# Kernel optimization log

Measured on AMD Instinct MI355X. Metric: run time of the kernel, lower is better.

## Reference

```python
import jax, jax.numpy as jnp
import numpy as np

B, N, D, K = 16, 1024, 512, 8
NUM_ITERS = 3
EPS = 1e-08
LN_EPS = 1e-05


def layer_norm(x, g, b):
    m = jnp.mean(x, axis=-1, keepdims=True)
    v = jnp.var(x, axis=-1, keepdims=True)
    return (x - m) * jax.lax.rsqrt(v + LN_EPS) * g + b


def setup_inputs() -> dict:
    key = jax.random.key(0)
    ks = jax.random.split(key, 8)
    s = 1.0 / np.sqrt(D)
    return {
        "embeddings": jax.random.normal(ks[0], (B, N, D), jnp.float32),
        "noise_init": jax.random.normal(ks[1], (B, K, D), jnp.float32),
        "noise_final": jax.random.normal(ks[2], (B, K, D), jnp.float32),
        "slots_mu": jax.random.normal(ks[3], (1, K, D), jnp.float32) * s,
        "slots_logsigma": jax.random.normal(ks[4], (1, K, D), jnp.float32) * s,
        "mixing_coeffs": jnp.ones((1, K), jnp.float32) / K,
        "Wk": jax.random.normal(ks[5], (D, D), jnp.float32) * s,
        "bk": jnp.zeros((D,), jnp.float32),
        "Wq": jax.random.normal(ks[6], (D, D), jnp.float32) * s,
        "bq": jnp.zeros((D,), jnp.float32),
        "Wv": jax.random.normal(ks[7], (D, D), jnp.float32) * s,
        "bv": jnp.zeros((D,), jnp.float32),
        "ln_g": jnp.ones((D,), jnp.float32),
        "ln_b": jnp.zeros((D,), jnp.float32),
    }


def reference(embeddings, noise_init, noise_final, slots_mu, slots_logsigma,
              mixing_coeffs, Wk, bk, Wq, bq, Wv, bv, ln_g, ln_b):
    b, n, d = embeddings.shape
    mixing = jnp.broadcast_to(mixing_coeffs, (b, K))           # [B,K]
    mu = jnp.broadcast_to(slots_mu, (b, K, d))                 # [B,K,D]
    sigma = jnp.exp(jnp.broadcast_to(slots_logsigma, (b, K, d)))
    slots = mu + sigma * noise_init                            # sampled slots

    x = layer_norm(embeddings, ln_g, ln_b)
    keys = x @ Wk + bk                                         # [B,N,D]
    values = x @ Wv + bv                                       # [B,N,D]
    # slots are never updated inside the loop, so queries are loop-invariant
    queries = slots @ Wq + bq                                  # [B,K,D]

    log2pi = jnp.float32(np.log(2.0 * np.pi))
    attn = None
    for _ in range(NUM_ITERS):
        diff = keys[:, :, None, :] - queries[:, None, :, :]    # [B,N,K,D]
        gll = -0.5 * jnp.sum(diff * diff / (sigma[:, None] ** 2 + EPS), axis=-1)  # [B,N,K]
        gll = (-0.5 * d * log2pi
               - 0.5 * jnp.sum(jnp.log(jnp.abs(sigma) + EPS), axis=-1)[:, None, :]
               + gll)
        attn = mixing[:, None, :] * gll                        # [B,N,K]
        attn = attn / jnp.sum(attn, axis=-1, keepdims=True)
        attn = attn / (jnp.sum(attn, axis=1, keepdims=True) + EPS)
        mu = jnp.einsum('bnk,bnd->bkd', attn, values)          # [B,K,D]
        diff2 = values[:, :, None, :] - mu[:, None, :, :]      # [B,N,K,D]
        sigma = jnp.einsum('bnk,bnkd->bkd', attn, diff2 * diff2)
        mixing = jnp.sum(attn, axis=1) / n

    sigma = jnp.maximum(jnp.abs(sigma), EPS)
    slots = mu + sigma * noise_final
    return slots, jnp.transpose(attn, (0, 2, 1))
```

## Files before the change

### kernel.cpp

```cpp
#include <hip/hip_runtime.h>
#include <math.h>

#define BB 16
#define NN 1024
#define DD 512
#define KK 8
#define EPS_ 1e-8f
#define LN_EPS_ 1e-5f
#define GLL_C0 (-470.4965290007924f)

typedef __attribute__((ext_vector_type(8))) short short8;
typedef __attribute__((ext_vector_type(4))) short short4v;
typedef __attribute__((ext_vector_type(4))) float f32x4;

static __device__ inline short f2bf(float f) {
    unsigned u = __builtin_bit_cast(unsigned, f);
    u = (u + 0x7fff + ((u >> 16) & 1)) >> 16;
    return (short)u;
}
static __device__ inline float bf2f(short s) {
    unsigned u = ((unsigned)(unsigned short)s) << 16;
    return __builtin_bit_cast(float, u);
}
static __device__ inline void gload16(const void* g, void* l) {
    __builtin_amdgcn_global_load_lds(
        (const __attribute__((address_space(1))) void*)g,
        (__attribute__((address_space(3))) void*)l, 16, 0, 0);
}

struct Params {
    const float *emb, *noise_init, *noise_final, *slots_mu, *slots_logsg,
                *mixing_co, *Wk, *bk, *Wq, *bq, *Wv, *bv, *ln_g, *ln_b;
    float *out;
    float *queries, *attn, *s1p, *s2p, *off, *mix16, *colsum;
    short *Abf, *E, *Vbf, *WtKV, *WqT, *slotbf, *F_bt;
};

__global__ __launch_bounds__(256) void k_pre(Params p)
{
    __shared__ __align__(16) short eb[4352];
    int u = blockIdx.x, tid = threadIdx.x;
    if (u < 4096) {
        int row  = u * 4 + (tid >> 6);
        int lane = tid & 63;
        const float* e = p.emb + (size_t)row * DD + lane * 8;
        float4 v0 = *(const float4*)e;
        float4 v1 = *(const float4*)(e + 4);
        float v[8] = {v0.x, v0.y, v0.z, v0.w, v1.x, v1.y, v1.z, v1.w};
        float s = 0.0f;
#pragma unroll
        for (int j = 0; j < 8; j++) s += v[j];
#pragma unroll
        for (int off = 32; off; off >>= 1) s += __shfl_xor(s, off);
        float m = s * (1.0f / DD);
        float vs = 0.0f;
#pragma unroll
        for (int j = 0; j < 8; j++) { float d = v[j] - m; vs = fmaf(d, d, vs); }
#pragma unroll
        for (int off = 32; off; off >>= 1) vs += __shfl_xor(vs, off);
        float rstd = rsqrtf(vs * (1.0f / DD) + LN_EPS_);

        float4 g0 = *(const float4*)&p.ln_g[lane * 8];
        float4 g1 = *(const float4*)&p.ln_g[lane * 8 + 4];
        float4 b0 = *(const float4*)&p.ln_b[lane * 8];
        float4 b1 = *(const float4*)&p.ln_b[lane * 8 + 4];
        float g[8] = {g0.x, g0.y, g0.z, g0.w, g1.x, g1.y, g1.z, g1.w};
        float bb[8] = {b0.x, b0.y, b0.z, b0.w, b1.x, b1.y, b1.z, b1.w};
        short8 o;
#pragma unroll
        for (int j = 0; j < 8; j++) o[j] = f2bf(fmaf((v[j] - m) * rstd, g[j], bb[j]));
        *(short8*)&p.Abf[(size_t)row * DD + lane * 8] = o;
    } else if (u < 4864) {
        int idx = u - 4096;
        int z = idx >> 8, rem = idx & 255;
        const float* W = (z == 0) ? p.Wk : (z == 1) ? p.Wv : p.Wq;
        short* T; int nbase;
        if (z < 2) { T = p.WtKV; nbase = z * 512; } else { T = p.WqT; nbase = 0; }
        int k0 = (rem & 15) * 32, n0 = (rem >> 4) * 32;
        int tx = tid & 31, ty = tid >> 5;
        float (*t)[33] = (float (*)[33])eb;
#pragma unroll
        for (int q = 0; q < 4; q++)
            t[ty + q * 8][tx] = W[(size_t)(k0 + ty + q * 8) * DD + n0 + tx];
        __syncthreads();
#pragma unroll
        for (int q = 0; q < 4; q++)
            T[(size_t)(nbase + n0 + ty + q * 8) * DD + k0 + tx] = f2bf(t[tx][ty + q * 8]);
    } else {
        int idx = u - 4864;
        int b = idx >> 3, k = idx & 7;
#pragma unroll
        for (int q = 0; q < 2; q++) {
            int d = tid + q * 256;
            float sg = expf(p.slots_logsg[k * DD + d]);
            float sl = fmaf(sg, p.noise_init[((size_t)(b * KK + k)) * DD + d],
                            p.slots_mu[k * DD + d]);
            p.slotbf[((size_t)(b * KK + k)) * DD + d] = f2bf(sl);
        }
    }
}

__global__ __launch_bounds__(256) void k_gemm(Params p)
{
    __shared__ __align__(16) short eb[128 * 128];
    int u = blockIdx.x, tid = threadIdx.x;
    int w = tid >> 6, l = tid & 63;
    int x = u & 7, by = u >> 3;
    int qmode = (by == 128);
    if (qmode && x >= 4) return;
    const short* A  = qmode ? p.slotbf : p.Abf + (size_t)by * 128 * DD;
    const short* Bt = qmode ? p.WqT : p.WtKV;
    int row0 = qmode ? 0 : by * 128;
    int col0 = x * 128;

    short* As = eb;
    short* Bs = eb + 8192;
    int sr = l >> 3;
    int sg_off = ((l & 7) ^ sr) * 8;
    int mq = (w & 1) * 64, nq = (w >> 1) * 64;
    int fr = l & 15;
    int orow = (l >> 4) * 4, ocol = l & 15;

    f32x4 acc[4][4] = {};
    for (int k0 = 0; k0 < DD; k0 += 64) {
        __syncthreads();
#pragma unroll
        for (int j = 0; j < 4; j++) {
            int rb = w * 32 + j * 8;
            int r  = rb + sr;
            gload16(A  + (size_t)r * DD + k0 + sg_off, &As[rb * 64 + l * 8]);
            gload16(Bt + (size_t)(col0 + r) * DD + k0 + sg_off, &Bs[rb * 64 + l * 8]);
        }
        __syncthreads();
#pragma unroll
        for (int kk = 0; kk < 2; kk++) {
            int g = kk * 4 + (l >> 4);
            short8 af[4], bfv[4];
#pragma unroll
            for (int mi = 0; mi < 4; mi++)
                af[mi] = *(const short8*)&As[(mq + mi * 16 + fr) * 64 + (g ^ (fr & 7)) * 8];
#pragma unroll
            for (int ni = 0; ni < 4; ni++)
                bfv[ni] = *(const short8*)&Bs[(nq + ni * 16 + fr) * 64 + (g ^ (fr & 7)) * 8];
#pragma unroll
            for (int mi = 0; mi < 4; mi++)
#pragma unroll
                for (int ni = 0; ni < 4; ni++)
                    acc[mi][ni] = __builtin_amdgcn_mfma_f32_16x16x32_bf16(
                        af[mi], bfv[ni], acc[mi][ni], 0, 0, 0);
        }
    }

    float bvv[4];
#pragma unroll
    for (int ni = 0; ni < 4; ni++) {
        int col = col0 + nq + ni * 16 + ocol;
        bvv[ni] = qmode ? p.bq[col] : (x < 4 ? p.bk[col] : p.bv[col - 512]);
    }

    __syncthreads();
    if (qmode) {
#pragma unroll
        for (int ni = 0; ni < 4; ni++) {
            int col = col0 + nq + ni * 16 + ocol;
#pragma unroll
            for (int mi = 0; mi < 4; mi++)
#pragma unroll
                for (int r = 0; r < 4; r++)
                    p.queries[(size_t)(mq + mi * 16 + orow + r) * DD + col] =
                        acc[mi][ni][r] + bvv[ni];
        }
    } else {
        int npass = (x < 4) ? 2 : 1;
        for (int pass = 0; pass < npass; pass++) {
#pragma unroll
            for (int mi = 0; mi < 4; mi++)
#pragma unroll
                for (int r = 0; r < 4; r++) {
                    int row = mq + mi * 16 + orow + r;
                    int sw = ((row >> 2) & 3) << 1;
#pragma unroll
                    for (int ni = 0; ni < 4; ni++) {
                        int colg = nq + ni * 16 + ocol;
                        float val = acc[mi][ni][r] + bvv[ni];
                        if (x < 4 && pass == 0) val = val * val;
                        eb[row * 128 + (((colg >> 3) ^ sw) * 8) + (colg & 7)] = f2bf(val);
                    }
                }
            __syncthreads();
#pragma unroll
            for (int i = 0; i < 8; i++) {
                int row = i * 16 + w * 4 + (l >> 4);
                int c = l & 15;
                int cc = c ^ (((row >> 2) & 3) << 1);
                short8 vv = *(const short8*)&eb[row * 128 + cc * 8];
                if (x < 4) {
                    size_t a = (size_t)(row0 + row) * 1024 +
                               (pass ? 512 + col0 : col0) + c * 8;
                    *(short8*)&p.E[a] = vv;
                } else {
                    *(short8*)&p.Vbf[(size_t)(row0 + row) * 512 +
                                     (col0 - 512) + c * 8] = vv;
                }
            }
            __syncthreads();
        }
    }
}

__global__ __launch_bounds__(256) void k_fprep0(Params p)
{
    __shared__ float red[512];
    int u = blockIdx.x, tid = threadIdx.x;
    int b = u >> 4, k = u & 15;
    short* Fr = p.F_bt + (size_t)(b * 16 + k) * 1024;
    if (k >= KK) {
        short4v zv = {0, 0, 0, 0};
        *(short4v*)&Fr[tid * 4] = zv;
        if (tid == 0) { p.off[b * 16 + k] = 0.0f; p.mix16[b * 16 + k] = 0.0f; }
        return;
    }
    float* rc = red;
    float* rl = red + 256;
    float c = 0.0f, ld = 0.0f;
#pragma unroll
    for (int q = 0; q < 2; q++) {
        int d = tid * 2 + q;
        float sg = expf(p.slots_logsg[k * DD + d]);
        float iv = 1.0f / (sg * sg + EPS_);
        float qv = p.queries[((size_t)(b * KK + k)) * DD + d];
        Fr[d]       = f2bf(-0.5f * iv);
        Fr[512 + d] = f2bf(qv * iv);
        c  = fmaf(qv * qv, iv, c);
        ld += logf(fabsf(sg) + EPS_);
    }
    rc[tid] = c; rl[tid] = ld;
    __syncthreads();
    for (int s = 128; s > 0; s >>= 1) {
        if (tid < s) { rc[tid] += rc[tid + s]; rl[tid] += rl[tid + s]; }
        __syncthreads();
    }
    if (tid == 0) {
        p.off[b * 16 + k]    = GLL_C0 - 0.5f * rl[0] - 0.5f * rc[0];
        p.mix16[b * 16 + k]  = p.mixing_co[k];
        p.colsum[b * KK + k] = 0.0f;
    }
}

__global__ __launch_bounds__(256) void k_gllmu(Params p)
{
    __shared__ float asml[64 * KK];
    int u = blockIdx.x, tid = threadIdx.x;
    int w = tid >> 6, l = tid & 63;
    int b = u >> 4, chunk = u & 15;
    int n0 = chunk * 64;
    int m0 = n0 + w * 16;

    const short* Ea = p.E + ((size_t)(b * NN + m0 + (l & 15))) * 1024 + (l >> 4) * 8;
    const short* Fa = p.F_bt + (size_t)(b * 16 + (l & 15)) * 1024 + (l >> 4) * 8;
    f32x4 acc = {};
#pragma unroll 8
    for (int j = 0; j < 32; j++) {
        short8 af = *(const short8*)&Ea[j * 32];
        short8 bf = *(const short8*)&Fa[j * 32];
        acc = __builtin_amdgcn_mfma_f32_16x16x32_bf16(af, bf, acc, 0, 0, 0);
    }
    int col = l & 15;
    int rloc = w * 16 + (l >> 4) * 4;
    float offv = p.off[b * 16 + col];
    float mixv = p.mix16[b * 16 + col];
    float a[4], den[4];
#pragma unroll
    for (int r = 0; r < 4; r++) {
        a[r] = mixv * (acc[r] + offv);
        den[r] = a[r];
    }
#pragma unroll
    for (int mask = 1; mask <= 8; mask <<= 1)
#pragma unroll
        for (int r = 0; r < 4; r++) den[r] += __shfl_xor(den[r], mask);
    float csl = 0.0f;
    if (col < KK) {
#pragma unroll
        for (int r = 0; r < 4; r++) {
            float vv = a[r] / den[r];
            asml[(rloc + r) * KK + col] = vv;
            p.attn[((size_t)(b * NN + n0 + rloc + r)) * KK + col] = vv;
            csl += vv;
        }
    }
    csl += __shfl_xor(csl, 16);
    csl += __shfl_xor(csl, 32);
    if (l < KK) atomicAdd(&p.colsum[b * KK + l], csl);

    __syncthreads();

    int d0 = tid * 2;
    float s1[2][KK] = {}, s2[2][KK] = {};
    const short* vb = p.Vbf + ((size_t)(b * NN + n0)) * DD + d0;
#pragma unroll 4
    for (int nn = 0; nn < 64; nn++) {
        short2 vs = *(const short2*)&vb[(size_t)nn * DD];
        float v0 = bf2f(vs.x), v1 = bf2f(vs.y);
        float v0q = v0 * v0, v1q = v1 * v1;
        float4 a0 = *(const float4*)&asml[nn * KK];
        float4 a1 = *(const float4*)&asml[nn * KK + 4];
        float aa[8] = {a0.x, a0.y, a0.z, a0.w, a1.x, a1.y, a1.z, a1.w};
#pragma unroll
        for (int k = 0; k < KK; k++) {
            s1[0][k] = fmaf(aa[k], v0, s1[0][k]);
            s2[0][k] = fmaf(aa[k], v0q, s2[0][k]);
            s1[1][k] = fmaf(aa[k], v1, s1[1][k]);
            s2[1][k] = fmaf(aa[k], v1q, s2[1][k]);
        }
    }
    size_t base = ((size_t)(b * 16 + chunk) * KK) * DD + d0;
#pragma unroll
    for (int k = 0; k < KK; k++) {
        *(float2*)&p.s1p[base + (size_t)k * DD] = make_float2(s1[0][k], s1[1][k]);
        *(float2*)&p.s2p[base + (size_t)k * DD] = make_float2(s2[0][k], s2[1][k]);
    }
}

__global__ __launch_bounds__(256) void k_fprep(Params p)
{
    __shared__ float red[512];
    int u = blockIdx.x, tid = threadIdx.x;
    int b = u >> 3, k = u & 7;
    float cs   = p.colsum[b * KK + k];
    float inv  = 1.0f / (cs + EPS_);
    float ssum = cs * inv;
    short* Fr = p.F_bt + (size_t)(b * 16 + k) * 1024;
    float* rc = red;
    float* rl = red + 256;
    float c = 0.0f, ld = 0.0f;
#pragma unroll
    for (int q = 0; q < 2; q++) {
        int d = tid * 2 + q;
        float s1 = 0.0f, s2 = 0.0f;
#pragma unroll
        for (int ns = 0; ns < 16; ns++) {
            size_t o = ((size_t)(b * 16 + ns) * KK + k) * DD + d;
            s1 += p.s1p[o];
            s2 += p.s2p[o];
        }
        float m  = s1 * inv;
        float sg = s2 * inv - m * m * (2.0f - ssum);
        float iv = 1.0f / (sg * sg + EPS_);
        float qv = p.queries[((size_t)(b * KK + k)) * DD + d];
        Fr[d]       = f2bf(-0.5f * iv);
        Fr[512 + d] = f2bf(qv * iv);
        c  = fmaf(qv * qv, iv, c);
        ld += logf(fabsf(sg) + EPS_);
    }
    rc[tid] = c; rl[tid] = ld;
    __syncthreads();
    for (int s = 128; s > 0; s >>= 1) {
        if (tid < s) { rc[tid] += rc[tid + s]; rl[tid] += rl[tid + s]; }
        __syncthreads();
    }
    if (tid == 0) {
        p.off[b * 16 + k]    = GLL_C0 - 0.5f * rl[0] - 0.5f * rc[0];
        p.mix16[b * 16 + k]  = ssum * (1.0f / NN);
        p.colsum[b * KK + k] = 0.0f;
    }
}

__global__ __launch_bounds__(256) void k_final(Params p)
{
    int u = blockIdx.x, tid = threadIdx.x;
    if (u < 256) {
        int gid = u * 256 + tid;
        int d = gid & 511;
        int k = (gid >> 9) & 7;
        int b = gid >> 12;
        float s1 = 0.0f, s2 = 0.0f;
#pragma unroll
        for (int ns = 0; ns < 16; ns++) {
            size_t o = ((size_t)(b * 16 + ns) * KK + k) * DD + d;
            s1 += p.s1p[o];
            s2 += p.s2p[o];
        }
        float cs   = p.colsum[b * KK + k];
        float inv  = 1.0f / (cs + EPS_);
        float ssum = cs * inv;
        float m    = s1 * inv;
        float sg   = s2 * inv - m * m * (2.0f - ssum);
        p.out[gid] = fmaf(fmaxf(fabsf(sg), EPS_), p.noise_final[gid], m);
    } else {
        int gid = (u - 256) * 256 + tid;
        int b = gid >> 13;
        int k = (gid >> 10) & 7;
        int n = gid & 1023;
        float cs = p.colsum[b * KK + k];
        p.out[BB * KK * DD + gid] =
            p.attn[((size_t)(b * NN + n)) * KK + k] / (cs + EPS_);
    }
}

extern "C" void kernel_launch(void* const* d_in, const int* in_sizes, int n_in,
                              void* d_out, int out_size, void* d_ws, size_t ws_size,
                              hipStream_t stream)
{
    Params pp;
    pp.emb         = (const float*)d_in[0];
    pp.noise_init  = (const float*)d_in[1];
    pp.noise_final = (const float*)d_in[2];
    pp.slots_mu    = (const float*)d_in[3];
    pp.slots_logsg = (const float*)d_in[4];
    pp.mixing_co   = (const float*)d_in[5];
    pp.Wk          = (const float*)d_in[6];
    pp.bk          = (const float*)d_in[7];
    pp.Wq          = (const float*)d_in[8];
    pp.bq          = (const float*)d_in[9];
    pp.Wv          = (const float*)d_in[10];
    pp.bv          = (const float*)d_in[11];
    pp.ln_g        = (const float*)d_in[12];
    pp.ln_b        = (const float*)d_in[13];
    pp.out         = (float*)d_out;

    float* ws = (float*)d_ws;
    pp.queries = ws;
    pp.attn    = pp.queries + BB * KK * DD;
    pp.s1p     = pp.attn + BB * NN * KK;
    pp.s2p     = pp.s1p + (size_t)BB * 16 * KK * DD;
    pp.off     = pp.s2p + (size_t)BB * 16 * KK * DD;
    pp.mix16   = pp.off + BB * 16;
    pp.colsum  = pp.mix16 + BB * 16;
    pp.Abf     = (short*)(pp.colsum + BB * KK);
    pp.E       = pp.Abf + (size_t)BB * NN * DD;
    pp.Vbf     = pp.E + (size_t)BB * NN * 1024;
    pp.WtKV    = pp.Vbf + (size_t)BB * NN * DD;
    pp.WqT     = pp.WtKV + (size_t)1024 * DD;
    pp.slotbf  = pp.WqT + (size_t)DD * DD;
    pp.F_bt    = pp.slotbf + (size_t)BB * KK * DD;

    k_pre<<<4992, 256, 0, stream>>>(pp);
    k_gemm<<<1032, 256, 0, stream>>>(pp);
    k_fprep0<<<256, 256, 0, stream>>>(pp);
    for (int it = 0; it < 3; it++) {
        k_gllmu<<<256, 256, 0, stream>>>(pp);
        if (it < 2) k_fprep<<<128, 256, 0, stream>>>(pp);
    }
    k_final<<<768, 256, 0, stream>>>(pp);
}
```

Before: 243.6 us.

## Double-buffer GEMM LDS tiles and split gll/mu kernel over more blocks

The projection GEMM now keeps two LDS buffers and issues the next K-tile's loads before computing on the current one, aiming to overlap global loads with MFMA work. The gll/mu kernel processes 32 rows per block instead of 64, with warp pairs splitting the 1024-long reduction and combining through shared memory. This doubles the block count for better GPU fill. In exchange, GEMM LDS use doubles (lower occupancy) and the downstream reductions read twice as many partial sums.

```diff
diff --git a/kernel.cpp b/kernel.cpp
--- a/kernel.cpp
+++ b/kernel.cpp
@@ -102,7 +102,7 @@
 
 __global__ __launch_bounds__(256) void k_gemm(Params p)
 {
-    __shared__ __align__(16) short eb[128 * 128];
+    __shared__ __align__(16) short smem[32768];
     int u = blockIdx.x, tid = threadIdx.x;
     int w = tid >> 6, l = tid & 63;
     int x = u & 7, by = u >> 3;
@@ -113,35 +113,42 @@
     int row0 = qmode ? 0 : by * 128;
     int col0 = x * 128;
 
-    short* As = eb;
-    short* Bs = eb + 8192;
     int sr = l >> 3;
     int sg_off = ((l & 7) ^ sr) * 8;
     int mq = (w & 1) * 64, nq = (w >> 1) * 64;
     int fr = l & 15;
     int orow = (l >> 4) * 4, ocol = l & 15;
 
+#define STAGE(buf, k0)                                                        \
+    {                                                                         \
+        short* As_ = smem + (buf) * 8192;                                     \
+        short* Bs_ = smem + 16384 + (buf) * 8192;                             \
+        _Pragma("unroll")                                                     \
+        for (int j = 0; j < 4; j++) {                                         \
+            int rb = w * 32 + j * 8;                                          \
+            int r  = rb + sr;                                                 \
+            gload16(A  + (size_t)r * DD + (k0) + sg_off, &As_[rb * 64 + l * 8]);   \
+            gload16(Bt + (size_t)(col0 + r) * DD + (k0) + sg_off, &Bs_[rb * 64 + l * 8]); \
+        }                                                                     \
+    }
+
     f32x4 acc[4][4] = {};
-    for (int k0 = 0; k0 < DD; k0 += 64) {
-        __syncthreads();
-#pragma unroll
-        for (int j = 0; j < 4; j++) {
-            int rb = w * 32 + j * 8;
-            int r  = rb + sr;
-            gload16(A  + (size_t)r * DD + k0 + sg_off, &As[rb * 64 + l * 8]);
-            gload16(Bt + (size_t)(col0 + r) * DD + k0 + sg_off, &Bs[rb * 64 + l * 8]);
-        }
-        __syncthreads();
+    STAGE(0, 0);
+    __syncthreads();
+    for (int i = 0; i < 8; i++) {
+        if (i < 7) STAGE((i + 1) & 1, (i + 1) * 64);
+        const short* As_ = smem + (i & 1) * 8192;
+        const short* Bs_ = smem + 16384 + (i & 1) * 8192;
 #pragma unroll
         for (int kk = 0; kk < 2; kk++) {
             int g = kk * 4 + (l >> 4);
             short8 af[4], bfv[4];
 #pragma unroll
             for (int mi = 0; mi < 4; mi++)
-                af[mi] = *(const short8*)&As[(mq + mi * 16 + fr) * 64 + (g ^ (fr & 7)) * 8];
+                af[mi] = *(const short8*)&As_[(mq + mi * 16 + fr) * 64 + (g ^ (fr & 7)) * 8];
 #pragma unroll
             for (int ni = 0; ni < 4; ni++)
-                bfv[ni] = *(const short8*)&Bs[(nq + ni * 16 + fr) * 64 + (g ^ (fr & 7)) * 8];
+                bfv[ni] = *(const short8*)&Bs_[(nq + ni * 16 + fr) * 64 + (g ^ (fr & 7)) * 8];
 #pragma unroll
             for (int mi = 0; mi < 4; mi++)
 #pragma unroll
@@ -149,7 +156,9 @@
                     acc[mi][ni] = __builtin_amdgcn_mfma_f32_16x16x32_bf16(
                         af[mi], bfv[ni], acc[mi][ni], 0, 0, 0);
         }
-    }
+        __syncthreads();
+    }
+#undef STAGE
 
     float bvv[4];
 #pragma unroll
@@ -158,7 +167,6 @@
         bvv[ni] = qmode ? p.bq[col] : (x < 4 ? p.bk[col] : p.bv[col - 512]);
     }
 
-    __syncthreads();
     if (qmode) {
 #pragma unroll
         for (int ni = 0; ni < 4; ni++) {
@@ -171,6 +179,7 @@
                         acc[mi][ni][r] + bvv[ni];
         }
     } else {
+        short* eb = smem;
         int npass = (x < 4) ? 2 : 1;
         for (int pass = 0; pass < npass; pass++) {
 #pragma unroll
@@ -249,57 +258,69 @@
 
 __global__ __launch_bounds__(256) void k_gllmu(Params p)
 {
-    __shared__ float asml[64 * KK];
+    __shared__ f32x4 red[2][64];
+    __shared__ float asml[32 * KK];
     int u = blockIdx.x, tid = threadIdx.x;
     int w = tid >> 6, l = tid & 63;
-    int b = u >> 4, chunk = u & 15;
-    int n0 = chunk * 64;
-    int m0 = n0 + w * 16;
-
-    const short* Ea = p.E + ((size_t)(b * NN + m0 + (l & 15))) * 1024 + (l >> 4) * 8;
-    const short* Fa = p.F_bt + (size_t)(b * 16 + (l & 15)) * 1024 + (l >> 4) * 8;
-    f32x4 acc = {};
-#pragma unroll 8
-    for (int j = 0; j < 32; j++) {
-        short8 af = *(const short8*)&Ea[j * 32];
-        short8 bf = *(const short8*)&Fa[j * 32];
-        acc = __builtin_amdgcn_mfma_f32_16x16x32_bf16(af, bf, acc, 0, 0, 0);
-    }
-    int col = l & 15;
-    int rloc = w * 16 + (l >> 4) * 4;
-    float offv = p.off[b * 16 + col];
-    float mixv = p.mix16[b * 16 + col];
-    float a[4], den[4];
-#pragma unroll
-    for (int r = 0; r < 4; r++) {
-        a[r] = mixv * (acc[r] + offv);
-        den[r] = a[r];
-    }
-#pragma unroll
-    for (int mask = 1; mask <= 8; mask <<= 1)
-#pragma unroll
-        for (int r = 0; r < 4; r++) den[r] += __shfl_xor(den[r], mask);
-    float csl = 0.0f;
-    if (col < KK) {
+    int b = u >> 5, chunk = u & 31;
+    int n0 = chunk * 32;
+    int t = w & 1, khalf = w >> 1;
+
+    const short* Ea = p.E + ((size_t)(b * NN + n0 + t * 16 + (l & 15))) * 1024
+                      + khalf * 512 + (l >> 4) * 8;
+    const short* Fa = p.F_bt + (size_t)(b * 16 + (l & 15)) * 1024
+                      + khalf * 512 + (l >> 4) * 8;
+    f32x4 acc0 = {}, acc1 = {};
+#pragma unroll
+    for (int j = 0; j < 8; j++) {
+        short8 a0 = *(const short8*)&Ea[j * 64];
+        short8 f0 = *(const short8*)&Fa[j * 64];
+        acc0 = __builtin_amdgcn_mfma_f32_16x16x32_bf16(a0, f0, acc0, 0, 0, 0);
+        short8 a1 = *(const short8*)&Ea[j * 64 + 32];
+        short8 f1 = *(const short8*)&Fa[j * 64 + 32];
+        acc1 = __builtin_amdgcn_mfma_f32_16x16x32_bf16(a1, f1, acc1, 0, 0, 0);
+    }
+    f32x4 acc = acc0 + acc1;
+
+    if (khalf) red[t][l] = acc;
+    __syncthreads();
+    if (!khalf) {
+        acc += red[t][l];
+        int col = l & 15;
+        int rloc = t * 16 + (l >> 4) * 4;
+        float offv = p.off[b * 16 + col];
+        float mixv = p.mix16[b * 16 + col];
+        float a[4], den[4];
 #pragma unroll
         for (int r = 0; r < 4; r++) {
-            float vv = a[r] / den[r];
-            asml[(rloc + r) * KK + col] = vv;
-            p.attn[((size_t)(b * NN + n0 + rloc + r)) * KK + col] = vv;
-            csl += vv;
-        }
-    }
-    csl += __shfl_xor(csl, 16);
-    csl += __shfl_xor(csl, 32);
-    if (l < KK) atomicAdd(&p.colsum[b * KK + l], csl);
-
+            a[r] = mixv * (acc[r] + offv);
+            den[r] = a[r];
+        }
+#pragma unroll
+        for (int mask = 1; mask <= 8; mask <<= 1)
+#pragma unroll
+            for (int r = 0; r < 4; r++) den[r] += __shfl_xor(den[r], mask);
+        float csl = 0.0f;
+        if (col < KK) {
+#pragma unroll
+            for (int r = 0; r < 4; r++) {
+                float vv = a[r] / den[r];
+                asml[(rloc + r) * KK + col] = vv;
+                p.attn[((size_t)(b * NN + n0 + rloc + r)) * KK + col] = vv;
+                csl += vv;
+            }
+        }
+        csl += __shfl_xor(csl, 16);
+        csl += __shfl_xor(csl, 32);
+        if (l < KK) atomicAdd(&p.colsum[b * KK + l], csl);
+    }
     __syncthreads();
 
     int d0 = tid * 2;
     float s1[2][KK] = {}, s2[2][KK] = {};
     const short* vb = p.Vbf + ((size_t)(b * NN + n0)) * DD + d0;
 #pragma unroll 4
-    for (int nn = 0; nn < 64; nn++) {
+    for (int nn = 0; nn < 32; nn++) {
         short2 vs = *(const short2*)&vb[(size_t)nn * DD];
         float v0 = bf2f(vs.x), v1 = bf2f(vs.y);
         float v0q = v0 * v0, v1q = v1 * v1;
@@ -314,7 +335,7 @@
             s2[1][k] = fmaf(aa[k], v1q, s2[1][k]);
         }
     }
-    size_t base = ((size_t)(b * 16 + chunk) * KK) * DD + d0;
+    size_t base = ((size_t)(b * 32 + chunk) * KK) * DD + d0;
 #pragma unroll
     for (int k = 0; k < KK; k++) {
         *(float2*)&p.s1p[base + (size_t)k * DD] = make_float2(s1[0][k], s1[1][k]);
@@ -339,8 +360,8 @@
         int d = tid * 2 + q;
         float s1 = 0.0f, s2 = 0.0f;
 #pragma unroll
-        for (int ns = 0; ns < 16; ns++) {
-            size_t o = ((size_t)(b * 16 + ns) * KK + k) * DD + d;
+        for (int ns = 0; ns < 32; ns++) {
+            size_t o = ((size_t)(b * 32 + ns) * KK + k) * DD + d;
             s1 += p.s1p[o];
             s2 += p.s2p[o];
         }
@@ -376,8 +397,8 @@
         int b = gid >> 12;
         float s1 = 0.0f, s2 = 0.0f;
 #pragma unroll
-        for (int ns = 0; ns < 16; ns++) {
-            size_t o = ((size_t)(b * 16 + ns) * KK + k) * DD + d;
+        for (int ns = 0; ns < 32; ns++) {
+            size_t o = ((size_t)(b * 32 + ns) * KK + k) * DD + d;
             s1 += p.s1p[o];
             s2 += p.s2p[o];
         }
@@ -423,8 +444,8 @@
     pp.queries = ws;
     pp.attn    = pp.queries + BB * KK * DD;
     pp.s1p     = pp.attn + BB * NN * KK;
-    pp.s2p     = pp.s1p + (size_t)BB * 16 * KK * DD;
-    pp.off     = pp.s2p + (size_t)BB * 16 * KK * DD;
+    pp.s2p     = pp.s1p + (size_t)BB * 32 * KK * DD;
+    pp.off     = pp.s2p + (size_t)BB * 32 * KK * DD;
     pp.mix16   = pp.off + BB * 16;
     pp.colsum  = pp.mix16 + BB * 16;
     pp.Abf     = (short*)(pp.colsum + BB * KK);
@@ -439,7 +460,7 @@
     k_gemm<<<1032, 256, 0, stream>>>(pp);
     k_fprep0<<<256, 256, 0, stream>>>(pp);
     for (int it = 0; it < 3; it++) {
-        k_gllmu<<<256, 256, 0, stream>>>(pp);
+        k_gllmu<<<512, 256, 0, stream>>>(pp);
         if (it < 2) k_fprep<<<128, 256, 0, stream>>>(pp);
     }
     k_final<<<768, 256, 0, stream>>>(pp);
```

After: 219.1 us. 1.11x faster.
